# Performance work log

Hardware: AMD Instinct MI355X
Metric: run time of the kernel (lower is better)

The kernel has to match this reference:

```python
import jax, jax.numpy as jnp
import numpy as np

COEFF = 0.95

def _combine(c1, c2):
    # linear recurrence element: x_n = a_n * x_{n-1} + b_n
    a1, b1 = c1
    a2, b2 = c2
    return (a1 * a2, a2 * b1 + b2)

def setup_inputs() -> dict:
    key = jax.random.key(0)
    inputs = jax.random.normal(key, (64, 480000), dtype=jnp.float32)
    return {"inputs": inputs}

def reference(inputs) -> jnp.ndarray:
    # x[0] = e[0]; x[n] = COEFF * x[n-1] + e[n]
    # Expressed as parallel (Blelloch) scan over pairs (a, b) with a == COEFF.
    # a[0]'s value is irrelevant since the implicit x[-1] = 0.
    a = jnp.full_like(inputs, COEFF)
    _, x = jax.lax.associative_scan(_combine, (a, inputs), axis=1)
    return x
```

## Files before the change

kernel.cpp:

```cpp
#include <hip/hip_runtime.h>


#define ROW_N   480000
#define TILE    4096
#define WARM    512
#define NTILES  ((ROW_N + TILE - 1) / TILE)
#define NROWS   64

__global__ __launch_bounds__(1024)
void deemph_kernel(const float* __restrict__ in, float* __restrict__ out) {
    const int row      = blockIdx.y;
    const int startcol = blockIdx.x * TILE;
    const int tid      = threadIdx.x;
    const int lane     = tid & 63;
    const int wave     = tid >> 6;

    const float* __restrict__ rin  = in  + (size_t)row * ROW_N;
    float*       __restrict__ rout = out + (size_t)row * ROW_N;

    __shared__ float warr[16];
    __shared__ float wsum[16];

    const float LOG2C = -0.07400058144377693f;

    float wpart = 0.0f;
    if (tid < WARM) {
        int col = startcol - WARM + tid;
        if (col >= 0) {
            float w = exp2f((float)(WARM - 1 - tid) * LOG2C);
            wpart = w * rin[col];
        }
    }
    #pragma unroll
    for (int d = 1; d < 64; d <<= 1)
        wpart += __shfl_xor(wpart, d, 64);

    const int col   = startcol + tid * 4;
    const bool valid = (col < ROW_N);
    float e0 = 0.f, e1 = 0.f, e2 = 0.f, e3 = 0.f;
    if (valid) {
        float4 v = *reinterpret_cast<const float4*>(rin + col);
        e0 = v.x; e1 = v.y; e2 = v.z; e3 = v.w;
    }
    float l0 = e0;
    float l1 = fmaf(0.95f, l0, e1);
    float l2 = fmaf(0.95f, l1, e2);
    float l3 = fmaf(0.95f, l2, e3);

    const float M0 = 0.81450625f;
    const float M1 = 0.66342043f;
    const float M2 = 0.44012667f;
    const float M3 = 0.19371148f;
    const float M4 = 0.03752413f;
    const float M5 = 0.00140806f;
    float b = l3;
    { float t = __shfl_up(b, 1,  64); if (lane >= 1)  b = fmaf(M0, t, b); }
    { float t = __shfl_up(b, 2,  64); if (lane >= 2)  b = fmaf(M1, t, b); }
    { float t = __shfl_up(b, 4,  64); if (lane >= 4)  b = fmaf(M2, t, b); }
    { float t = __shfl_up(b, 8,  64); if (lane >= 8)  b = fmaf(M3, t, b); }
    { float t = __shfl_up(b, 16, 64); if (lane >= 16) b = fmaf(M4, t, b); }
    { float t = __shfl_up(b, 32, 64); if (lane >= 32) b = fmaf(M5, t, b); }

    float excl = __shfl_up(b, 1, 64);
    if (lane == 0) excl = 0.0f;

    if (lane == 63) warr[wave] = b;
    if (lane == 0)  wsum[wave] = wpart;
    __syncthreads();

    const float C256 = 1.9826347e-06f;
    float E = 0.0f;
    for (int u = 0; u < wave; ++u) E = fmaf(E, C256, warr[u]);
    float carry_warm = 0.0f;
    #pragma unroll
    for (int u = 0; u < 16; ++u) carry_warm += wsum[u];

    float pw = exp2f((float)(256 * wave) * LOG2C);
    float Sw = fmaf(pw, carry_warm, E);
    float pl = exp2f((float)(4 * lane) * LOG2C);
    float Q  = fmaf(pl, Sw, excl);

    if (valid) {
        float4 r;
        r.x = fmaf(0.95f,       Q, l0);
        r.y = fmaf(0.9025f,     Q, l1);
        r.z = fmaf(0.857375f,   Q, l2);
        r.w = fmaf(0.81450625f, Q, l3);
        *reinterpret_cast<float4*>(rout + col) = r;
    }
}

extern "C" void kernel_launch(void* const* d_in, const int* in_sizes, int n_in,
                              void* d_out, int out_size, void* d_ws, size_t ws_size,
                              hipStream_t stream) {
    const float* in = (const float*)d_in[0];
    float* out = (float*)d_out;
    dim3 grid(NTILES, NROWS);
    deemph_kernel<<<grid, 1024, 0, stream>>>(in, out);
}
```

Measured before the change: 47.32 us.

## Double tile width to eight elements per thread with vectorized warmup and nontemporal stores

Doubles the tile size so each thread processes eight consecutive elements, and rescales the wave-scan decay constants and cross-wave carry to match. This halves the number of tiles and with it the share of redundant warmup-window reads per output element. The warmup sum now uses 128 threads that each load a float4 and partially combine it, and outputs are written with nontemporal stores. In exchange each thread holds more registers, and the grid shrinks to fewer, larger blocks, which can reduce occupancy or worsen load balance.

```diff
diff --git a/kernel.cpp b/kernel.cpp
--- a/kernel.cpp
+++ b/kernel.cpp
@@ -2,10 +2,12 @@
 
 
 #define ROW_N   480000
-#define TILE    4096
+#define TILE    8192
 #define WARM    512
 #define NTILES  ((ROW_N + TILE - 1) / TILE)
 #define NROWS   64
+
+typedef float vfloat4 __attribute__((ext_vector_type(4)));
 
 __global__ __launch_bounds__(1024)
 void deemph_kernel(const float* __restrict__ in, float* __restrict__ out) {
@@ -24,36 +26,44 @@
     const float LOG2C = -0.07400058144377693f;
 
     float wpart = 0.0f;
-    if (tid < WARM) {
-        int col = startcol - WARM + tid;
-        if (col >= 0) {
-            float w = exp2f((float)(WARM - 1 - tid) * LOG2C);
-            wpart = w * rin[col];
-        }
+    if (startcol > 0 && tid < (WARM / 4)) {
+        int wcol = startcol - WARM + tid * 4;
+        vfloat4 v = *reinterpret_cast<const vfloat4*>(rin + wcol);
+        float s = v.w;
+        s = fmaf(0.95f,     v.z, s);
+        s = fmaf(0.9025f,   v.y, s);
+        s = fmaf(0.857375f, v.x, s);
+        wpart = exp2f((float)(WARM - 4 - 4 * tid) * LOG2C) * s;
     }
     #pragma unroll
     for (int d = 1; d < 64; d <<= 1)
         wpart += __shfl_xor(wpart, d, 64);
 
-    const int col   = startcol + tid * 4;
+    const int col    = startcol + tid * 8;
     const bool valid = (col < ROW_N);
-    float e0 = 0.f, e1 = 0.f, e2 = 0.f, e3 = 0.f;
+    float e0=0.f,e1=0.f,e2=0.f,e3=0.f,e4=0.f,e5=0.f,e6=0.f,e7=0.f;
     if (valid) {
-        float4 v = *reinterpret_cast<const float4*>(rin + col);
-        e0 = v.x; e1 = v.y; e2 = v.z; e3 = v.w;
+        vfloat4 va = *reinterpret_cast<const vfloat4*>(rin + col);
+        vfloat4 vb = *reinterpret_cast<const vfloat4*>(rin + col + 4);
+        e0=va.x; e1=va.y; e2=va.z; e3=va.w;
+        e4=vb.x; e5=vb.y; e6=vb.z; e7=vb.w;
     }
     float l0 = e0;
     float l1 = fmaf(0.95f, l0, e1);
     float l2 = fmaf(0.95f, l1, e2);
     float l3 = fmaf(0.95f, l2, e3);
+    float l4 = fmaf(0.95f, l3, e4);
+    float l5 = fmaf(0.95f, l4, e5);
+    float l6 = fmaf(0.95f, l5, e6);
+    float l7 = fmaf(0.95f, l6, e7);
 
-    const float M0 = 0.81450625f;
-    const float M1 = 0.66342043f;
-    const float M2 = 0.44012667f;
-    const float M3 = 0.19371148f;
-    const float M4 = 0.03752413f;
-    const float M5 = 0.00140806f;
-    float b = l3;
+    const float M0 = 0.66342043f;
+    const float M1 = 0.44012667f;
+    const float M2 = 0.19371148f;
+    const float M3 = 0.03752413f;
+    const float M4 = 0.00140806f;
+    const float M5 = 1.9826347e-06f;
+    float b = l7;
     { float t = __shfl_up(b, 1,  64); if (lane >= 1)  b = fmaf(M0, t, b); }
     { float t = __shfl_up(b, 2,  64); if (lane >= 2)  b = fmaf(M1, t, b); }
     { float t = __shfl_up(b, 4,  64); if (lane >= 4)  b = fmaf(M2, t, b); }
@@ -68,25 +78,30 @@
     if (lane == 0)  wsum[wave] = wpart;
     __syncthreads();
 
-    const float C256 = 1.9826347e-06f;
+    const float C512 = 3.930483e-12f;
     float E = 0.0f;
-    for (int u = 0; u < wave; ++u) E = fmaf(E, C256, warr[u]);
+    for (int u = 0; u < wave; ++u) E = fmaf(E, C512, warr[u]);
     float carry_warm = 0.0f;
     #pragma unroll
     for (int u = 0; u < 16; ++u) carry_warm += wsum[u];
 
-    float pw = exp2f((float)(256 * wave) * LOG2C);
+    float pw = exp2f((float)(512 * wave) * LOG2C);
     float Sw = fmaf(pw, carry_warm, E);
-    float pl = exp2f((float)(4 * lane) * LOG2C);
+    float pl = exp2f((float)(8 * lane) * LOG2C);
     float Q  = fmaf(pl, Sw, excl);
 
     if (valid) {
-        float4 r;
-        r.x = fmaf(0.95f,       Q, l0);
-        r.y = fmaf(0.9025f,     Q, l1);
-        r.z = fmaf(0.857375f,   Q, l2);
-        r.w = fmaf(0.81450625f, Q, l3);
-        *reinterpret_cast<float4*>(rout + col) = r;
+        vfloat4 ra, rb;
+        ra.x = fmaf(0.95f,               Q, l0);
+        ra.y = fmaf(0.9025f,             Q, l1);
+        ra.z = fmaf(0.857375f,           Q, l2);
+        ra.w = fmaf(0.81450625f,         Q, l3);
+        rb.x = fmaf(0.7737809375f,       Q, l4);
+        rb.y = fmaf(0.735091890625f,     Q, l5);
+        rb.z = fmaf(0.69833729609375f,   Q, l6);
+        rb.w = fmaf(0.6634204312890625f, Q, l7);
+        __builtin_nontemporal_store(ra, reinterpret_cast<vfloat4*>(rout + col));
+        __builtin_nontemporal_store(rb, reinterpret_cast<vfloat4*>(rout + col + 4));
     }
 }
 
```

After: 54.30 us. 1.15x slower.
